# Optimization experiments

Measured on AMD Instinct MI355X. Metric: run time of the kernel, lower is better.

Reference implementation:

```python
import jax, jax.numpy as jnp
import numpy as np

EPS = 1e-3  # tfa InstanceNormalization default epsilon
H = 4       # num_attention_heads


def _inorm(x, g, b, axes):
    # instance norm: normalize over the given (spatial) axes, affine per channel
    m = jnp.mean(x, axis=axes, keepdims=True)
    v = jnp.var(x, axis=axes, keepdims=True)
    return (x - m) * jax.lax.rsqrt(v + EPS) * g + b


def setup_inputs() -> dict:
    key = jax.random.key(0)
    ks = jax.random.split(key, 20)
    B, N, C, E = 1, 196, 480, 4  # batch, tokens, KV_size_C, embedding_channels
    d = {}
    for i, n in enumerate(['emb1', 'emb2', 'emb3', 'emb4']):
        d[n] = jax.random.normal(ks[i], (B, N, E), jnp.float32)
    d['emb_C'] = jax.random.normal(ks[4], (B, N, C), jnp.float32)
    for i, n in enumerate(['Wq_C', 'Wk_C', 'Wv_C']):
        d[n] = jax.random.normal(ks[5 + i], (C, C), jnp.float32) * 0.02
    for i, n in enumerate(['Wq1', 'Wq2', 'Wq3', 'Wq4', 'Wk', 'Wv', 'Wo1', 'Wo2', 'Wo3', 'Wo4']):
        d[n] = jax.random.normal(ks[8 + i], (E, E), jnp.float32) * 0.25
    d['g1'] = jnp.ones((), jnp.float32)   # psi1 gamma (single channel)
    d['b1'] = jnp.zeros((), jnp.float32)  # psi1 beta
    d['g2'] = jnp.ones((H,), jnp.float32)   # psi2 gamma (per head)
    d['b2'] = jnp.zeros((H,), jnp.float32)  # psi2 beta
    return d


def reference(emb1, emb2, emb3, emb4, emb_C, Wq_C, Wk_C, Wv_C,
              Wq1, Wq2, Wq3, Wq4, Wk, Wv, Wo1, Wo2, Wo3, Wo4,
              g1, b1, g2, b2):
    B, N, C = emb_C.shape
    # ---- channel attention over emb_C ----
    Qc = emb_C @ Wq_C
    Kc = emb_C @ Wk_C
    Vc = emb_C @ Wv_C
    attn = jnp.einsum('bnc,bnd->bcd', Qc, Kc)            # Q_C^T @ K_C  [B,C,C]
    attn = _inorm(attn, g1, b1, axes=(-2, -1))           # psi1: 1-channel instance norm
    sim = jax.nn.softmax(attn, axis=-1)                  # dropout inactive (inference)
    T_hat = jnp.einsum('bcd,bnd->bnc', sim, Vc)          # (sim @ V_C^T)^T  [B,N,C]
    # split into C//4 chunks of width 4 along channels, concat along tokens
    KV_S = T_hat.reshape(B, N, C // 4, 4).transpose(0, 2, 1, 3).reshape(B, (C // 4) * N, 4)

    def heads(x):  # [B,T,4] -> [B,H,T,1]
        return x.reshape(B, -1, H, 1).transpose(0, 2, 1, 3)

    K = heads(KV_S @ Wk)   # [B,H,M,1], M = N*C//4
    V = heads(KV_S @ Wv)
    gh = g2.reshape(1, H, 1, 1)
    bh = b2.reshape(1, H, 1, 1)

    def branch(emb, Wq, Wo):
        Q = heads(emb @ Wq)                                  # [B,H,Nq,1]
        a = jnp.einsum('bhqd,bhkd->bhqk', Q, K)              # [B,H,Nq,M]
        a = _inorm(a, gh, bh, axes=(-2, -1))                 # psi2: per-head instance norm
        a = jax.nn.softmax(a, axis=-1)
        c = jnp.einsum('bhqk,bhkd->bhqd', a, V)              # [B,H,Nq,1]
        c = c.transpose(0, 2, 1, 3).reshape(B, -1, H)        # [B,Nq,4] (= KV_size_S)
        return c @ Wo

    return (branch(emb1, Wq1, Wo1), branch(emb2, Wq2, Wo2),
            branch(emb3, Wq3, Wo3), branch(emb4, Wq4, Wo4))
```

## Files before the change

### kernel.cpp

```cpp
#include <hip/hip_runtime.h>
#include <hip/hip_bf16.h>
#include <math.h>

#define N_TOK 196
#define M_KV  23520
#define EPSN  1e-3f
#define LOG2E 1.44269504088896340736f

#define OFF_QC    0
#define OFF_KC    94080
#define OFF_VC    188160
#define OFF_ATTN  282240
#define OFF_KV    512640
#define OFF_SPART 700800
#define OFF_KPART 701056

__device__ __forceinline__ float fast_exp2(float x) {
#if __has_builtin(__builtin_amdgcn_exp2f)
    return __builtin_amdgcn_exp2f(x);
#else
    return exp2f(x);
#endif
}

#define GEMM_COMPUTE(AS, BS) \
    _Pragma("unroll") \
    for (int kk2 = 0; kk2 < 16; ++kk2) { \
        float4 av = *(const float4*)&AS[kk2][ty*4]; \
        float2 bv = *(const float2*)&BS[kk2][tx*2]; \
        a00 = fmaf(av.x, bv.x, a00); a01 = fmaf(av.x, bv.y, a01); \
        a10 = fmaf(av.y, bv.x, a10); a11 = fmaf(av.y, bv.y, a11); \
        a20 = fmaf(av.z, bv.x, a20); a21 = fmaf(av.z, bv.y, a21); \
        a30 = fmaf(av.w, bv.x, a30); a31 = fmaf(av.w, bv.y, a31); \
    }

#define COMBINE_ACCS(CMB) \
    if (kg == 1) { \
        CMB[ty*4+0][tx*2] = a00; CMB[ty*4+0][tx*2+1] = a01; \
        CMB[ty*4+1][tx*2] = a10; CMB[ty*4+1][tx*2+1] = a11; \
        CMB[ty*4+2][tx*2] = a20; CMB[ty*4+2][tx*2+1] = a21; \
        CMB[ty*4+3][tx*2] = a30; CMB[ty*4+3][tx*2+1] = a31; \
    } \
    __syncthreads(); \
    if (kg == 0) { \
        a00 += CMB[ty*4+0][tx*2]; a01 += CMB[ty*4+0][tx*2+1]; \
        a10 += CMB[ty*4+1][tx*2]; a11 += CMB[ty*4+1][tx*2+1]; \
        a20 += CMB[ty*4+2][tx*2]; a21 += CMB[ty*4+2][tx*2+1]; \
        a30 += CMB[ty*4+3][tx*2]; a31 += CMB[ty*4+3][tx*2+1]; \
    }

__global__ __launch_bounds__(512) void k_qkv(const float* __restrict__ embC,
                                             const float* __restrict__ Wq,
                                             const float* __restrict__ Wk,
                                             const float* __restrict__ Wv,
                                             float* __restrict__ ws) {
    int bid = blockIdx.x;
    int zi = bid / 60, rem = bid % 60;
    int m0 = (rem / 15) * 64, n0 = (rem % 15) * 32;
    const float* W = (zi == 0) ? Wq : (zi == 1 ? Wk : Wv);
    float* o = ws + zi * 94080;
    __shared__ float As[2][2][16][68];
    __shared__ float Bs[2][2][16][36];
    __shared__ float Cmb[64][33];
    int tid = threadIdx.x;
    int kg = tid >> 8, t = tid & 255;
    int ty = t >> 4, tx = t & 15;
    float a00=0,a01=0,a10=0,a11=0,a20=0,a21=0,a30=0,a31=0;
    const float4 z4 = make_float4(0,0,0,0);
    int mrow = t >> 2, kq = (t & 3) * 4;
    bool am = (m0 + mrow) < N_TOK;
    const float* aptr = embC + (m0 + mrow) * 480 + kg * 240 + kq;
    bool bact = t < 128;
    int kk = t >> 3, nq = (t & 7) * 4;
    const float* bptr = W + (kg * 240 + kk) * 480 + n0 + nq;
    const int NS = 15;
    float4 ra = am ? *(const float4*)(aptr) : z4;
    float4 rb = bact ? *(const float4*)(bptr) : z4;
    As[kg][0][kq+0][mrow]=ra.x; As[kg][0][kq+1][mrow]=ra.y;
    As[kg][0][kq+2][mrow]=ra.z; As[kg][0][kq+3][mrow]=ra.w;
    if (bact) *(float4*)&Bs[kg][0][kk][nq] = rb;
    ra = am ? *(const float4*)(aptr + 16) : z4;
    rb = bact ? *(const float4*)(bptr + 16*480) : z4;
    __syncthreads();
    for (int s = 0; s < NS; ++s) {
        int b = s & 1;
        float4 fa = z4, fb = z4;
        if (s + 2 < NS) {
            fa = am ? *(const float4*)(aptr + (s+2)*16) : z4;
            fb = bact ? *(const float4*)(bptr + (s+2)*16*480) : z4;
        }
        GEMM_COMPUTE(As[kg][b], Bs[kg][b]);
        if (s + 1 < NS) {
            int nb = b ^ 1;
            As[kg][nb][kq+0][mrow]=ra.x; As[kg][nb][kq+1][mrow]=ra.y;
            As[kg][nb][kq+2][mrow]=ra.z; As[kg][nb][kq+3][mrow]=ra.w;
            if (bact) *(float4*)&Bs[kg][nb][kk][nq] = rb;
        }
        __syncthreads();
        ra = fa; rb = fb;
    }
    COMBINE_ACCS(Cmb);
    if (kg == 0) {
        int m = m0 + ty*4, n = n0 + tx*2;
        if (m   < N_TOK) *(float2*)(o + (m  )*480 + n) = make_float2(a00, a01);
        if (m+1 < N_TOK) *(float2*)(o + (m+1)*480 + n) = make_float2(a10, a11);
        if (m+2 < N_TOK) *(float2*)(o + (m+2)*480 + n) = make_float2(a20, a21);
        if (m+3 < N_TOK) *(float2*)(o + (m+3)*480 + n) = make_float2(a30, a31);
    }
}

__global__ __launch_bounds__(512) void k_attn(const float* __restrict__ Qc,
                                              const float* __restrict__ Kc,
                                              float* __restrict__ attn,
                                              float* __restrict__ Spart) {
    __shared__ float As[2][2][16][68];
    __shared__ float Bs[2][2][16][36];
    __shared__ float Cmb[64][33];
    __shared__ float red[8][2];
    int tid = threadIdx.x;
    int kg = tid >> 8, t = tid & 255;
    int n0 = blockIdx.x * 32, m0 = blockIdx.y * 64;
    int ty = t >> 4, tx = t & 15;
    float a00=0,a01=0,a10=0,a11=0,a20=0,a21=0,a30=0,a31=0;
    const float4 z4 = make_float4(0,0,0,0);
    int kka = t >> 4, mq = (t & 15) * 4;
    bool amq = (m0 + mq) < 480;
    int kbase = kg * 112;
    const float* aptr = Qc + (kbase + kka) * 480 + m0 + mq;
    bool bact = t < 128;
    int kk = t >> 3, nq = (t & 7) * 4;
    const float* bptr = Kc + (kbase + kk) * 480 + n0 + nq;
    const int NS = 7;
    float4 ra = (amq && kbase + kka < N_TOK) ? *(const float4*)(aptr) : z4;
    float4 rb = (bact && kbase + kk < N_TOK) ? *(const float4*)(bptr) : z4;
    *(float4*)&As[kg][0][kka][mq] = ra;
    if (bact) *(float4*)&Bs[kg][0][kk][nq] = rb;
    ra = (amq && kbase + 16 + kka < N_TOK) ? *(const float4*)(aptr + 16*480) : z4;
    rb = (bact && kbase + 16 + kk < N_TOK) ? *(const float4*)(bptr + 16*480) : z4;
    __syncthreads();
    for (int s = 0; s < NS; ++s) {
        int b = s & 1;
        float4 fa = z4, fb = z4;
        if (s + 2 < NS) {
            int k0 = kbase + (s + 2) * 16;
            fa = (amq && k0 + kka < N_TOK) ? *(const float4*)(aptr + (s+2)*16*480) : z4;
            fb = (bact && k0 + kk < N_TOK) ? *(const float4*)(bptr + (s+2)*16*480) : z4;
        }
        GEMM_COMPUTE(As[kg][b], Bs[kg][b]);
        if (s + 1 < NS) {
            int nb = b ^ 1;
            *(float4*)&As[kg][nb][kka][mq] = ra;
            if (bact) *(float4*)&Bs[kg][nb][kk][nq] = rb;
        }
        __syncthreads();
        ra = fa; rb = fb;
    }
    COMBINE_ACCS(Cmb);
    float ls = 0.f, lq = 0.f;
    if (kg == 0) {
        int m = m0 + ty*4, n = n0 + tx*2;
        if (m   < 480) *(float2*)(attn + (m  )*480 + n) = make_float2(a00, a01);
        if (m+1 < 480) *(float2*)(attn + (m+1)*480 + n) = make_float2(a10, a11);
        if (m+2 < 480) *(float2*)(attn + (m+2)*480 + n) = make_float2(a20, a21);
        if (m+3 < 480) *(float2*)(attn + (m+3)*480 + n) = make_float2(a30, a31);
        ls = a00+a01+a10+a11+a20+a21+a30+a31;
        lq = a00*a00+a01*a01+a10*a10+a11*a11+a20*a20+a21*a21+a30*a30+a31*a31;
    }
    #pragma unroll
    for (int o = 32; o > 0; o >>= 1) { ls += __shfl_xor(ls, o, 64); lq += __shfl_xor(lq, o, 64); }
    int wid = tid >> 6, lane = tid & 63;
    if (lane == 0) { red[wid][0] = ls; red[wid][1] = lq; }
    __syncthreads();
    if (tid == 0) {
        int bid = blockIdx.y * gridDim.x + blockIdx.x;
        Spart[bid*2]   = red[0][0] + red[1][0] + red[2][0] + red[3][0];
        Spart[bid*2+1] = red[0][1] + red[1][1] + red[2][1] + red[3][1];
    }
}

__global__ __launch_bounds__(512) void k_thatkv(const float* __restrict__ Vc,
                                                const float* __restrict__ attn,
                                                const float* __restrict__ Spart,
                                                const float* __restrict__ g1,
                                                const float* __restrict__ Wk,
                                                const float* __restrict__ Wv,
                                                float2* __restrict__ KV,
                                                float* __restrict__ kpart) {
    __shared__ float As[2][2][16][68];
    __shared__ float Bs[2][2][16][36];
    __shared__ float red[8][16];
    __shared__ float colsum[32];
    __shared__ float Tile[64][33];
    int bid = blockIdx.x;
    int n0 = (bid % 15) * 32, m0 = (bid / 15) * 64;
    int tid = threadIdx.x;
    int kg = tid >> 8, t = tid & 255;
    int wid = tid >> 6, lane = tid & 63;
    if (tid < 32) colsum[tid] = 0.f;
    float ps = 0.f, pq = 0.f;
    if (tid < 120) { ps = Spart[tid*2]; pq = Spart[tid*2+1]; }
    #pragma unroll
    for (int o = 32; o > 0; o >>= 1) { ps += __shfl_xor(ps, o, 64); pq += __shfl_xor(pq, o, 64); }
    if (lane == 0) { red[wid][0] = ps; red[wid][1] = pq; }
    __syncthreads();
    float S = 0.f, SQ = 0.f;
    #pragma unroll
    for (int w = 0; w < 8; ++w) { S += red[w][0]; SQ += red[w][1]; }
    const float invCC = 1.f / (480.f * 480.f);
    float mean = S * invCC;
    float var  = SQ * invCC - mean * mean;
    float s2 = g1[0] * rsqrtf(var + EPSN) * LOG2E;
    int ty = t >> 4, tx = t & 15;
    float a00=0,a01=0,a10=0,a11=0,a20=0,a21=0,a30=0,a31=0;
    const float4 z4 = make_float4(0,0,0,0);
    int mrow = t >> 2, kq = (t & 3) * 4;
    bool am = (m0 + mrow) < N_TOK;
    const float* aptr = Vc + (m0 + mrow) * 480 + kg * 240 + kq;
    bool bact = t < 128;
    int nrow = t >> 2, bkq = (t & 3) * 4;
    const float* bptr = attn + (n0 + nrow) * 480 + kg * 240 + bkq;
    float bsum = 0.f;
    const int NS = 15;
    float4 ra = am ? *(const float4*)(aptr) : z4;
    float4 rb = bact ? *(const float4*)(bptr) : z4;
    As[kg][0][kq+0][mrow]=ra.x; As[kg][0][kq+1][mrow]=ra.y;
    As[kg][0][kq+2][mrow]=ra.z; As[kg][0][kq+3][mrow]=ra.w;
    if (bact) {
        float e0 = fast_exp2(s2 * rb.x), e1 = fast_exp2(s2 * rb.y);
        float e2 = fast_exp2(s2 * rb.z), e3 = fast_exp2(s2 * rb.w);
        Bs[kg][0][bkq+0][nrow] = e0; Bs[kg][0][bkq+1][nrow] = e1;
        Bs[kg][0][bkq+2][nrow] = e2; Bs[kg][0][bkq+3][nrow] = e3;
        bsum += e0 + e1 + e2 + e3;
    }
    ra = am ? *(const float4*)(aptr + 16) : z4;
    rb = bact ? *(const float4*)(bptr + 16) : z4;
    __syncthreads();
    for (int s = 0; s < NS; ++s) {
        int b = s & 1;
        float4 fa = z4, fb = z4;
        if (s + 2 < NS) {
            fa = am ? *(const float4*)(aptr + (s+2)*16) : z4;
            fb = bact ? *(const float4*)(bptr + (s+2)*16) : z4;
        }
        GEMM_COMPUTE(As[kg][b], Bs[kg][b]);
        if (s + 1 < NS) {
            int nb = b ^ 1;
            As[kg][nb][kq+0][mrow]=ra.x; As[kg][nb][kq+1][mrow]=ra.y;
            As[kg][nb][kq+2][mrow]=ra.z; As[kg][nb][kq+3][mrow]=ra.w;
            if (bact) {
                float e0 = fast_exp2(s2 * rb.x), e1 = fast_exp2(s2 * rb.y);
                float e2 = fast_exp2(s2 * rb.z), e3 = fast_exp2(s2 * rb.w);
                Bs[kg][nb][bkq+0][nrow] = e0; Bs[kg][nb][bkq+1][nrow] = e1;
                Bs[kg][nb][bkq+2][nrow] = e2; Bs[kg][nb][bkq+3][nrow] = e3;
                bsum += e0 + e1 + e2 + e3;
            }
        }
        __syncthreads();
        ra = fa; rb = fb;
    }
    if (bact) atomicAdd(&colsum[nrow], bsum);
    __syncthreads();
    if (tid < 32) colsum[tid] = 1.f / colsum[tid];
    int r0 = ty*4, cc = tx*2;
    if (kg == 1) {
        Tile[r0+0][cc] = a00; Tile[r0+0][cc+1] = a01;
        Tile[r0+1][cc] = a10; Tile[r0+1][cc+1] = a11;
        Tile[r0+2][cc] = a20; Tile[r0+2][cc+1] = a21;
        Tile[r0+3][cc] = a30; Tile[r0+3][cc+1] = a31;
    }
    __syncthreads();
    if (kg == 0) {
        float i0 = colsum[cc], i1 = colsum[cc+1];
        Tile[r0+0][cc] = (Tile[r0+0][cc] + a00) * i0; Tile[r0+0][cc+1] = (Tile[r0+0][cc+1] + a01) * i1;
        Tile[r0+1][cc] = (Tile[r0+1][cc] + a10) * i0; Tile[r0+1][cc+1] = (Tile[r0+1][cc+1] + a11) * i1;
        Tile[r0+2][cc] = (Tile[r0+2][cc] + a20) * i0; Tile[r0+2][cc+1] = (Tile[r0+2][cc+1] + a21) * i1;
        Tile[r0+3][cc] = (Tile[r0+3][cc] + a30) * i0; Tile[r0+3][cc+1] = (Tile[r0+3][cc+1] + a31) * i1;
    }
    __syncthreads();
    float su[4] = {0,0,0,0}, sq[4] = {0,0,0,0};
    {
        int e = tid;
        int tr = e >> 3, jj = e & 7;
        int tok = m0 + tr;
        bool act = tok < N_TOK;
        float c0 = Tile[tr][4*jj], c1 = Tile[tr][4*jj+1];
        float c2 = Tile[tr][4*jj+2], c3 = Tile[tr][4*jj+3];
        int m_kv = (n0/4 + jj) * 196 + tok;
        #pragma unroll
        for (int h = 0; h < 4; ++h) {
            float kh = c0*Wk[h] + c1*Wk[4+h] + c2*Wk[8+h] + c3*Wk[12+h];
            float vh = c0*Wv[h] + c1*Wv[4+h] + c2*Wv[8+h] + c3*Wv[12+h];
            if (act) {
                KV[h * M_KV + m_kv] = make_float2(kh, vh);
                su[h] += kh; sq[h] += kh * kh;
            }
        }
    }
    __syncthreads();
    #pragma unroll
    for (int h = 0; h < 4; ++h) {
        #pragma unroll
        for (int o = 32; o > 0; o >>= 1) {
            su[h] += __shfl_xor(su[h], o, 64);
            sq[h] += __shfl_xor(sq[h], o, 64);
        }
        if (lane == 0) { red[wid][h*2+0] = su[h]; red[wid][h*2+1] = sq[h]; }
    }
    __syncthreads();
    if (tid < 8) {
        int h = tid & 3, st = tid >> 2;
        float r = 0.f;
        #pragma unroll
        for (int w = 0; w < 8; ++w) r += red[w][h*2+st];
        kpart[st * 256 + h * 64 + bid] = r;
    }
}

#define QG 49
__global__ __launch_bounds__(1024) void k_branch(
        const float* __restrict__ emb1, const float* __restrict__ emb2,
        const float* __restrict__ emb3, const float* __restrict__ emb4,
        const float* __restrict__ Wq1, const float* __restrict__ Wq2,
        const float* __restrict__ Wq3, const float* __restrict__ Wq4,
        const float* __restrict__ g2v,
        const float2* __restrict__ KV, const float* __restrict__ kpart,
        const float* __restrict__ Wo1, const float* __restrict__ Wo2,
        const float* __restrict__ Wo3, const float* __restrict__ Wo4,
        float* __restrict__ out) {
    __shared__ float lsh[4][4][4];
    __shared__ float ash[4][4][4];
    int tid = threadIdx.x;
    int w = tid >> 6, lane = tid & 63;
    int h = w >> 2, p = w & 3;
    int bid = blockIdx.x;
    int i = bid / QG, qg = bid % QG;
    const float* emb = (i == 0) ? emb1 : (i == 1) ? emb2 : (i == 2) ? emb3 : emb4;
    const float* Wq  = (i == 0) ? Wq1 : (i == 1) ? Wq2 : (i == 2) ? Wq3 : Wq4;
    float wq0 = Wq[h], wq1 = Wq[4+h], wq2 = Wq[8+h], wq3 = Wq[12+h];
    float s = 0.f, s2 = 0.f;
    #pragma unroll
    for (int r = 0; r < 4; ++r) {
        int t = lane + r * 64;
        if (t < N_TOK) {
            float Q = emb[t*4]*wq0 + emb[t*4+1]*wq1 + emb[t*4+2]*wq2 + emb[t*4+3]*wq3;
            s += Q; s2 += Q * Q;
        }
    }
    float ks = 0.f, kq2 = 0.f;
    if (lane < 60) {
        ks  = kpart[0*256 + h*64 + lane];
        kq2 = kpart[1*256 + h*64 + lane];
    }
    #pragma unroll
    for (int o = 32; o > 0; o >>= 1) {
        s += __shfl_xor(s, o, 64); s2 += __shfl_xor(s2, o, 64);
        ks += __shfl_xor(ks, o, 64); kq2 += __shfl_xor(kq2, o, 64);
    }
    float Qbar = s * (1.f/196.f), Q2bar = s2 * (1.f/196.f);
    float Kbar = ks * (1.f/(float)M_KV), K2bar = kq2 * (1.f/(float)M_KV);
    float mu = Qbar * Kbar;
    float var = Q2bar * K2bar - mu * mu;
    float sc = g2v[h] * rsqrtf(var + EPSN);
    float B2[4];
    #pragma unroll
    for (int j = 0; j < 4; ++j) {
        int q = qg * 4 + j;
        float Qj = emb[q*4]*wq0 + emb[q*4+1]*wq1 + emb[q*4+2]*wq2 + emb[q*4+3]*wq3;
        B2[j] = Qj * sc * LOG2E;
    }
    const float4* kv4 = (const float4*)(KV + h * M_KV);
    const int KQ = M_KV / 8;
    int kstart = p * KQ, kendq = kstart + KQ;
    float l[4] = {0,0,0,0};
    float a[4] = {0,0,0,0};
#define PROC8(P) { \
        _Pragma("unroll") \
        for (int j = 0; j < 4; ++j) { \
            float x = fast_exp2(B2[j] * P.x); \
            l[j] += x; a[j] = fmaf(x, P.y, a[j]); \
            float y = fast_exp2(B2[j] * P.z); \
            l[j] += y; a[j] = fmaf(y, P.w, a[j]); \
        } }
    int k4 = kstart + lane;
    for (; k4 + 192 < kendq; k4 += 256) {
        float4 p0 = kv4[k4], p1 = kv4[k4+64], p2 = kv4[k4+128], p3 = kv4[k4+192];
        PROC8(p0); PROC8(p1); PROC8(p2); PROC8(p3);
    }
    for (; k4 < kendq; k4 += 64) { float4 pv = kv4[k4]; PROC8(pv); }
#undef PROC8
    #pragma unroll
    for (int j = 0; j < 4; ++j) {
        float lv = l[j], av = a[j];
        #pragma unroll
        for (int o = 32; o > 0; o >>= 1) { lv += __shfl_xor(lv, o, 64); av += __shfl_xor(av, o, 64); }
        if (lane == 0) { lsh[h][p][j] = lv; ash[h][p][j] = av; }
    }
    __syncthreads();
    if (tid < 4) {
        const float* Wo = (i == 0) ? Wo1 : (i == 1) ? Wo2 : (i == 2) ? Wo3 : Wo4;
        int j = tid;
        float c[4];
        #pragma unroll
        for (int hh = 0; hh < 4; ++hh) {
            float L = lsh[hh][0][j] + lsh[hh][1][j] + lsh[hh][2][j] + lsh[hh][3][j];
            float A = ash[hh][0][j] + ash[hh][1][j] + ash[hh][2][j] + ash[hh][3][j];
            c[hh] = A / L;
        }
        float4 o;
        o.x = c[0]*Wo[0] + c[1]*Wo[4] + c[2]*Wo[8]  + c[3]*Wo[12];
        o.y = c[0]*Wo[1] + c[1]*Wo[5] + c[2]*Wo[9]  + c[3]*Wo[13];
        o.z = c[0]*Wo[2] + c[1]*Wo[6] + c[2]*Wo[10] + c[3]*Wo[14];
        o.w = c[0]*Wo[3] + c[1]*Wo[7] + c[2]*Wo[11] + c[3]*Wo[15];
        *(float4*)(out + i * 784 + (qg * 4 + j) * 4) = o;
    }
}

extern "C" void kernel_launch(void* const* d_in, const int* in_sizes, int n_in,
                              void* d_out, int out_size, void* d_ws, size_t ws_size,
                              hipStream_t stream) {
    const float* emb1 = (const float*)d_in[0];
    const float* emb2 = (const float*)d_in[1];
    const float* emb3 = (const float*)d_in[2];
    const float* emb4 = (const float*)d_in[3];
    const float* embC = (const float*)d_in[4];
    const float* WqC  = (const float*)d_in[5];
    const float* WkC  = (const float*)d_in[6];
    const float* WvC  = (const float*)d_in[7];
    const float* Wq1  = (const float*)d_in[8];
    const float* Wq2  = (const float*)d_in[9];
    const float* Wq3  = (const float*)d_in[10];
    const float* Wq4  = (const float*)d_in[11];
    const float* Wk   = (const float*)d_in[12];
    const float* Wv   = (const float*)d_in[13];
    const float* Wo1  = (const float*)d_in[14];
    const float* Wo2  = (const float*)d_in[15];
    const float* Wo3  = (const float*)d_in[16];
    const float* Wo4  = (const float*)d_in[17];
    const float* g1   = (const float*)d_in[18];
    const float* g2   = (const float*)d_in[20];
    float* ws = (float*)d_ws;
    float* out = (float*)d_out;

    k_qkv<<<180, 512, 0, stream>>>(embC, WqC, WkC, WvC, ws);
    k_attn<<<dim3(15, 8), 512, 0, stream>>>(ws + OFF_QC, ws + OFF_KC,
                                            ws + OFF_ATTN, ws + OFF_SPART);
    k_thatkv<<<60, 512, 0, stream>>>(ws + OFF_VC, ws + OFF_ATTN, ws + OFF_SPART, g1,
                                     Wk, Wv, (float2*)(ws + OFF_KV), ws + OFF_KPART);
    k_branch<<<4 * QG, 1024, 0, stream>>>(emb1, emb2, emb3, emb4,
                                          Wq1, Wq2, Wq3, Wq4, g2,
                                          (const float2*)(ws + OFF_KV), ws + OFF_KPART,
                                          Wo1, Wo2, Wo3, Wo4, out);
}
```

Baseline: 64.87 us.

## Shrink attn and T_hat GEMM tiles to 32x32 to launch more blocks

The channel-attention GEMM and the T_hat/KV GEMM now use 32x32 output tiles with 2x2 per-thread micro-tiles instead of 64x32 with 4x2. This raises block counts from 120 to 225 and from 60 to 105, so more of the GPU's compute units are busy on these small problems. Partial-sum buffers, the workspace offsets and the reduction readers in k_thatkv and k_branch are resized to match. In exchange each thread does less work per shared-memory load and per-block sync, and the global loads are narrower.

```diff
diff --git a/kernel.cpp b/kernel.cpp
--- a/kernel.cpp
+++ b/kernel.cpp
@@ -13,7 +13,7 @@
 #define OFF_ATTN  282240
 #define OFF_KV    512640
 #define OFF_SPART 700800
-#define OFF_KPART 701056
+#define OFF_KPART 701312
 
 __device__ __forceinline__ float fast_exp2(float x) {
 #if __has_builtin(__builtin_amdgcn_exp2f)
@@ -23,7 +23,7 @@
 #endif
 }
 
-#define GEMM_COMPUTE(AS, BS) \
+#define GEMM_COMPUTE8(AS, BS) \
     _Pragma("unroll") \
     for (int kk2 = 0; kk2 < 16; ++kk2) { \
         float4 av = *(const float4*)&AS[kk2][ty*4]; \
@@ -34,19 +34,13 @@
         a30 = fmaf(av.w, bv.x, a30); a31 = fmaf(av.w, bv.y, a31); \
     }
 
-#define COMBINE_ACCS(CMB) \
-    if (kg == 1) { \
-        CMB[ty*4+0][tx*2] = a00; CMB[ty*4+0][tx*2+1] = a01; \
-        CMB[ty*4+1][tx*2] = a10; CMB[ty*4+1][tx*2+1] = a11; \
-        CMB[ty*4+2][tx*2] = a20; CMB[ty*4+2][tx*2+1] = a21; \
-        CMB[ty*4+3][tx*2] = a30; CMB[ty*4+3][tx*2+1] = a31; \
-    } \
-    __syncthreads(); \
-    if (kg == 0) { \
-        a00 += CMB[ty*4+0][tx*2]; a01 += CMB[ty*4+0][tx*2+1]; \
-        a10 += CMB[ty*4+1][tx*2]; a11 += CMB[ty*4+1][tx*2+1]; \
-        a20 += CMB[ty*4+2][tx*2]; a21 += CMB[ty*4+2][tx*2+1]; \
-        a30 += CMB[ty*4+3][tx*2]; a31 += CMB[ty*4+3][tx*2+1]; \
+#define GEMM_COMPUTE4(AS, BS) \
+    _Pragma("unroll") \
+    for (int kk2 = 0; kk2 < 16; ++kk2) { \
+        float2 av = *(const float2*)&AS[kk2][ty*2]; \
+        float2 bv = *(const float2*)&BS[kk2][tx*2]; \
+        a00 = fmaf(av.x, bv.x, a00); a01 = fmaf(av.x, bv.y, a01); \
+        a10 = fmaf(av.y, bv.x, a10); a11 = fmaf(av.y, bv.y, a11); \
     }
 
 __global__ __launch_bounds__(512) void k_qkv(const float* __restrict__ embC,
@@ -89,7 +83,7 @@
             fa = am ? *(const float4*)(aptr + (s+2)*16) : z4;
             fb = bact ? *(const float4*)(bptr + (s+2)*16*480) : z4;
         }
-        GEMM_COMPUTE(As[kg][b], Bs[kg][b]);
+        GEMM_COMPUTE8(As[kg][b], Bs[kg][b]);
         if (s + 1 < NS) {
             int nb = b ^ 1;
             As[kg][nb][kq+0][mrow]=ra.x; As[kg][nb][kq+1][mrow]=ra.y;
@@ -99,8 +93,18 @@
         __syncthreads();
         ra = fa; rb = fb;
     }
-    COMBINE_ACCS(Cmb);
+    if (kg == 1) {
+        Cmb[ty*4+0][tx*2] = a00; Cmb[ty*4+0][tx*2+1] = a01;
+        Cmb[ty*4+1][tx*2] = a10; Cmb[ty*4+1][tx*2+1] = a11;
+        Cmb[ty*4+2][tx*2] = a20; Cmb[ty*4+2][tx*2+1] = a21;
+        Cmb[ty*4+3][tx*2] = a30; Cmb[ty*4+3][tx*2+1] = a31;
+    }
+    __syncthreads();
     if (kg == 0) {
+        a00 += Cmb[ty*4+0][tx*2]; a01 += Cmb[ty*4+0][tx*2+1];
+        a10 += Cmb[ty*4+1][tx*2]; a11 += Cmb[ty*4+1][tx*2+1];
+        a20 += Cmb[ty*4+2][tx*2]; a21 += Cmb[ty*4+2][tx*2+1];
+        a30 += Cmb[ty*4+3][tx*2]; a31 += Cmb[ty*4+3][tx*2+1];
         int m = m0 + ty*4, n = n0 + tx*2;
         if (m   < N_TOK) *(float2*)(o + (m  )*480 + n) = make_float2(a00, a01);
         if (m+1 < N_TOK) *(float2*)(o + (m+1)*480 + n) = make_float2(a10, a11);
@@ -113,58 +117,62 @@
                                               const float* __restrict__ Kc,
                                               float* __restrict__ attn,
                                               float* __restrict__ Spart) {
-    __shared__ float As[2][2][16][68];
+    __shared__ float As[2][2][16][36];
     __shared__ float Bs[2][2][16][36];
-    __shared__ float Cmb[64][33];
+    __shared__ float Cmb[32][33];
     __shared__ float red[8][2];
     int tid = threadIdx.x;
     int kg = tid >> 8, t = tid & 255;
-    int n0 = blockIdx.x * 32, m0 = blockIdx.y * 64;
+    int n0 = blockIdx.x * 32, m0 = blockIdx.y * 32;
     int ty = t >> 4, tx = t & 15;
-    float a00=0,a01=0,a10=0,a11=0,a20=0,a21=0,a30=0,a31=0;
-    const float4 z4 = make_float4(0,0,0,0);
-    int kka = t >> 4, mq = (t & 15) * 4;
-    bool amq = (m0 + mq) < 480;
+    float a00=0,a01=0,a10=0,a11=0;
+    const float2 z2 = make_float2(0,0);
+    int kk = t >> 4, eq = (t & 15) * 2;
     int kbase = kg * 112;
-    const float* aptr = Qc + (kbase + kka) * 480 + m0 + mq;
-    bool bact = t < 128;
-    int kk = t >> 3, nq = (t & 7) * 4;
-    const float* bptr = Kc + (kbase + kk) * 480 + n0 + nq;
+    const float* aptr = Qc + kk * 480 + m0 + eq;
+    const float* bptr = Kc + kk * 480 + n0 + eq;
     const int NS = 7;
-    float4 ra = (amq && kbase + kka < N_TOK) ? *(const float4*)(aptr) : z4;
-    float4 rb = (bact && kbase + kk < N_TOK) ? *(const float4*)(bptr) : z4;
-    *(float4*)&As[kg][0][kka][mq] = ra;
-    if (bact) *(float4*)&Bs[kg][0][kk][nq] = rb;
-    ra = (amq && kbase + 16 + kka < N_TOK) ? *(const float4*)(aptr + 16*480) : z4;
-    rb = (bact && kbase + 16 + kk < N_TOK) ? *(const float4*)(bptr + 16*480) : z4;
+    float2 ra = (kbase + kk < N_TOK) ? *(const float2*)(aptr + kbase*480) : z2;
+    float2 rb = (kbase + kk < N_TOK) ? *(const float2*)(bptr + kbase*480) : z2;
+    *(float2*)&As[kg][0][kk][eq] = ra;
+    *(float2*)&Bs[kg][0][kk][eq] = rb;
+    bool v1 = (kbase + 16 + kk) < N_TOK;
+    ra = v1 ? *(const float2*)(aptr + (kbase+16)*480) : z2;
+    rb = v1 ? *(const float2*)(bptr + (kbase+16)*480) : z2;
     __syncthreads();
     for (int s = 0; s < NS; ++s) {
         int b = s & 1;
-        float4 fa = z4, fb = z4;
+        float2 fa = z2, fb = z2;
         if (s + 2 < NS) {
             int k0 = kbase + (s + 2) * 16;
-            fa = (amq && k0 + kka < N_TOK) ? *(const float4*)(aptr + (s+2)*16*480) : z4;
-            fb = (bact && k0 + kk < N_TOK) ? *(const float4*)(bptr + (s+2)*16*480) : z4;
-        }
-        GEMM_COMPUTE(As[kg][b], Bs[kg][b]);
+            if (k0 + kk < N_TOK) {
+                fa = *(const float2*)(aptr + k0*480);
+                fb = *(const float2*)(bptr + k0*480);
+            }
+        }
+        GEMM_COMPUTE4(As[kg][b], Bs[kg][b]);
         if (s + 1 < NS) {
             int nb = b ^ 1;
-            *(float4*)&As[kg][nb][kka][mq] = ra;
-            if (bact) *(float4*)&Bs[kg][nb][kk][nq] = rb;
+            *(float2*)&As[kg][nb][kk][eq] = ra;
+            *(float2*)&Bs[kg][nb][kk][eq] = rb;
         }
         __syncthreads();
         ra = fa; rb = fb;
     }
-    COMBINE_ACCS(Cmb);
+    if (kg == 1) {
+        Cmb[ty*2+0][tx*2] = a00; Cmb[ty*2+0][tx*2+1] = a01;
+        Cmb[ty*2+1][tx*2] = a10; Cmb[ty*2+1][tx*2+1] = a11;
+    }
+    __syncthreads();
     float ls = 0.f, lq = 0.f;
     if (kg == 0) {
-        int m = m0 + ty*4, n = n0 + tx*2;
-        if (m   < 480) *(float2*)(attn + (m  )*480 + n) = make_float2(a00, a01);
-        if (m+1 < 480) *(float2*)(attn + (m+1)*480 + n) = make_float2(a10, a11);
-        if (m+2 < 480) *(float2*)(attn + (m+2)*480 + n) = make_float2(a20, a21);
-        if (m+3 < 480) *(float2*)(attn + (m+3)*480 + n) = make_float2(a30, a31);
-        ls = a00+a01+a10+a11+a20+a21+a30+a31;
-        lq = a00*a00+a01*a01+a10*a10+a11*a11+a20*a20+a21*a21+a30*a30+a31*a31;
+        a00 += Cmb[ty*2+0][tx*2]; a01 += Cmb[ty*2+0][tx*2+1];
+        a10 += Cmb[ty*2+1][tx*2]; a11 += Cmb[ty*2+1][tx*2+1];
+        int m = m0 + ty*2, n = n0 + tx*2;
+        *(float2*)(attn + (m  )*480 + n) = make_float2(a00, a01);
+        *(float2*)(attn + (m+1)*480 + n) = make_float2(a10, a11);
+        ls = a00+a01+a10+a11;
+        lq = a00*a00+a01*a01+a10*a10+a11*a11;
     }
     #pragma unroll
     for (int o = 32; o > 0; o >>= 1) { ls += __shfl_xor(ls, o, 64); lq += __shfl_xor(lq, o, 64); }
@@ -173,8 +181,11 @@
     __syncthreads();
     if (tid == 0) {
         int bid = blockIdx.y * gridDim.x + blockIdx.x;
-        Spart[bid*2]   = red[0][0] + red[1][0] + red[2][0] + red[3][0];
-        Spart[bid*2+1] = red[0][1] + red[1][1] + red[2][1] + red[3][1];
+        float S = 0.f, SQ = 0.f;
+        #pragma unroll
+        for (int w = 0; w < 8; ++w) { S += red[w][0]; SQ += red[w][1]; }
+        Spart[bid*2]   = S;
+        Spart[bid*2+1] = SQ;
     }
 }
 
@@ -186,101 +197,88 @@
                                                 const float* __restrict__ Wv,
                                                 float2* __restrict__ KV,
                                                 float* __restrict__ kpart) {
-    __shared__ float As[2][2][16][68];
+    __shared__ float As[2][2][16][36];
     __shared__ float Bs[2][2][16][36];
-    __shared__ float red[8][16];
+    __shared__ float Cmb[32][33];
+    __shared__ float Tile[32][33];
+    __shared__ float red[8][8];
     __shared__ float colsum[32];
-    __shared__ float Tile[64][33];
     int bid = blockIdx.x;
-    int n0 = (bid % 15) * 32, m0 = (bid / 15) * 64;
+    int n0 = (bid % 15) * 32, m0 = (bid / 15) * 32;
     int tid = threadIdx.x;
     int kg = tid >> 8, t = tid & 255;
     int wid = tid >> 6, lane = tid & 63;
     if (tid < 32) colsum[tid] = 0.f;
     float ps = 0.f, pq = 0.f;
-    if (tid < 120) { ps = Spart[tid*2]; pq = Spart[tid*2+1]; }
+    if (tid < 225) { ps = Spart[tid*2]; pq = Spart[tid*2+1]; }
     #pragma unroll
     for (int o = 32; o > 0; o >>= 1) { ps += __shfl_xor(ps, o, 64); pq += __shfl_xor(pq, o, 64); }
-    if (lane == 0) { red[wid][0] = ps; red[wid][1] = pq; }
+    __shared__ float pr[8][2];
+    if (lane == 0) { pr[wid][0] = ps; pr[wid][1] = pq; }
     __syncthreads();
     float S = 0.f, SQ = 0.f;
     #pragma unroll
-    for (int w = 0; w < 8; ++w) { S += red[w][0]; SQ += red[w][1]; }
+    for (int w = 0; w < 8; ++w) { S += pr[w][0]; SQ += pr[w][1]; }
     const float invCC = 1.f / (480.f * 480.f);
     float mean = S * invCC;
     float var  = SQ * invCC - mean * mean;
     float s2 = g1[0] * rsqrtf(var + EPSN) * LOG2E;
     int ty = t >> 4, tx = t & 15;
-    float a00=0,a01=0,a10=0,a11=0,a20=0,a21=0,a30=0,a31=0;
-    const float4 z4 = make_float4(0,0,0,0);
-    int mrow = t >> 2, kq = (t & 3) * 4;
-    bool am = (m0 + mrow) < N_TOK;
-    const float* aptr = Vc + (m0 + mrow) * 480 + kg * 240 + kq;
-    bool bact = t < 128;
-    int nrow = t >> 2, bkq = (t & 3) * 4;
-    const float* bptr = attn + (n0 + nrow) * 480 + kg * 240 + bkq;
+    float a00=0,a01=0,a10=0,a11=0;
+    const float2 z2 = make_float2(0,0);
+    int mm = t >> 3, kq2 = (t & 7) * 2;
+    bool am = (m0 + mm) < N_TOK;
+    const float* aptr = Vc + (m0 + mm) * 480 + kg * 240 + kq2;
+    const float* bptr = attn + (n0 + mm) * 480 + kg * 240 + kq2;
     float bsum = 0.f;
     const int NS = 15;
-    float4 ra = am ? *(const float4*)(aptr) : z4;
-    float4 rb = bact ? *(const float4*)(bptr) : z4;
-    As[kg][0][kq+0][mrow]=ra.x; As[kg][0][kq+1][mrow]=ra.y;
-    As[kg][0][kq+2][mrow]=ra.z; As[kg][0][kq+3][mrow]=ra.w;
-    if (bact) {
+    float2 ra = am ? *(const float2*)(aptr) : z2;
+    float2 rb = *(const float2*)(bptr);
+    As[kg][0][kq2][mm] = ra.x; As[kg][0][kq2+1][mm] = ra.y;
+    {
         float e0 = fast_exp2(s2 * rb.x), e1 = fast_exp2(s2 * rb.y);
-        float e2 = fast_exp2(s2 * rb.z), e3 = fast_exp2(s2 * rb.w);
-        Bs[kg][0][bkq+0][nrow] = e0; Bs[kg][0][bkq+1][nrow] = e1;
-        Bs[kg][0][bkq+2][nrow] = e2; Bs[kg][0][bkq+3][nrow] = e3;
-        bsum += e0 + e1 + e2 + e3;
-    }
-    ra = am ? *(const float4*)(aptr + 16) : z4;
-    rb = bact ? *(const float4*)(bptr + 16) : z4;
+        Bs[kg][0][kq2][mm] = e0; Bs[kg][0][kq2+1][mm] = e1;
+        bsum += e0 + e1;
+    }
+    ra = am ? *(const float2*)(aptr + 16) : z2;
+    rb = *(const float2*)(bptr + 16);
     __syncthreads();
     for (int s = 0; s < NS; ++s) {
         int b = s & 1;
-        float4 fa = z4, fb = z4;
+        float2 fa = z2, fb = z2;
         if (s + 2 < NS) {
-            fa = am ? *(const float4*)(aptr + (s+2)*16) : z4;
-            fb = bact ? *(const float4*)(bptr + (s+2)*16) : z4;
-        }
-        GEMM_COMPUTE(As[kg][b], Bs[kg][b]);
+            fa = am ? *(const float2*)(aptr + (s+2)*16) : z2;
+            fb = *(const float2*)(bptr + (s+2)*16);
+        }
+        GEMM_COMPUTE4(As[kg][b], Bs[kg][b]);
         if (s + 1 < NS) {
             int nb = b ^ 1;
-            As[kg][nb][kq+0][mrow]=ra.x; As[kg][nb][kq+1][mrow]=ra.y;
-            As[kg][nb][kq+2][mrow]=ra.z; As[kg][nb][kq+3][mrow]=ra.w;
-            if (bact) {
-                float e0 = fast_exp2(s2 * rb.x), e1 = fast_exp2(s2 * rb.y);
-                float e2 = fast_exp2(s2 * rb.z), e3 = fast_exp2(s2 * rb.w);
-                Bs[kg][nb][bkq+0][nrow] = e0; Bs[kg][nb][bkq+1][nrow] = e1;
-                Bs[kg][nb][bkq+2][nrow] = e2; Bs[kg][nb][bkq+3][nrow] = e3;
-                bsum += e0 + e1 + e2 + e3;
-            }
+            As[kg][nb][kq2][mm] = ra.x; As[kg][nb][kq2+1][mm] = ra.y;
+            float e0 = fast_exp2(s2 * rb.x), e1 = fast_exp2(s2 * rb.y);
+            Bs[kg][nb][kq2][mm] = e0; Bs[kg][nb][kq2+1][mm] = e1;
+            bsum += e0 + e1;
         }
         __syncthreads();
         ra = fa; rb = fb;
     }
-    if (bact) atomicAdd(&colsum[nrow], bsum);
+    atomicAdd(&colsum[mm], bsum);
+    int r0 = ty*2, cc = tx*2;
+    if (kg == 1) {
+        Cmb[r0+0][cc] = a00; Cmb[r0+0][cc+1] = a01;
+        Cmb[r0+1][cc] = a10; Cmb[r0+1][cc+1] = a11;
+    }
     __syncthreads();
     if (tid < 32) colsum[tid] = 1.f / colsum[tid];
-    int r0 = ty*4, cc = tx*2;
-    if (kg == 1) {
-        Tile[r0+0][cc] = a00; Tile[r0+0][cc+1] = a01;
-        Tile[r0+1][cc] = a10; Tile[r0+1][cc+1] = a11;
-        Tile[r0+2][cc] = a20; Tile[r0+2][cc+1] = a21;
-        Tile[r0+3][cc] = a30; Tile[r0+3][cc+1] = a31;
-    }
     __syncthreads();
     if (kg == 0) {
         float i0 = colsum[cc], i1 = colsum[cc+1];
-        Tile[r0+0][cc] = (Tile[r0+0][cc] + a00) * i0; Tile[r0+0][cc+1] = (Tile[r0+0][cc+1] + a01) * i1;
-        Tile[r0+1][cc] = (Tile[r0+1][cc] + a10) * i0; Tile[r0+1][cc+1] = (Tile[r0+1][cc+1] + a11) * i1;
-        Tile[r0+2][cc] = (Tile[r0+2][cc] + a20) * i0; Tile[r0+2][cc+1] = (Tile[r0+2][cc+1] + a21) * i1;
-        Tile[r0+3][cc] = (Tile[r0+3][cc] + a30) * i0; Tile[r0+3][cc+1] = (Tile[r0+3][cc+1] + a31) * i1;
+        Tile[r0+0][cc] = (Cmb[r0+0][cc] + a00) * i0; Tile[r0+0][cc+1] = (Cmb[r0+0][cc+1] + a01) * i1;
+        Tile[r0+1][cc] = (Cmb[r0+1][cc] + a10) * i0; Tile[r0+1][cc+1] = (Cmb[r0+1][cc+1] + a11) * i1;
     }
     __syncthreads();
     float su[4] = {0,0,0,0}, sq[4] = {0,0,0,0};
-    {
-        int e = tid;
-        int tr = e >> 3, jj = e & 7;
+    if (tid < 256) {
+        int tr = tid >> 3, jj = tid & 7;
         int tok = m0 + tr;
         bool act = tok < N_TOK;
         float c0 = Tile[tr][4*jj], c1 = Tile[tr][4*jj+1];
@@ -312,7 +310,7 @@
         float r = 0.f;
         #pragma unroll
         for (int w = 0; w < 8; ++w) r += red[w][h*2+st];
-        kpart[st * 256 + h * 64 + bid] = r;
+        kpart[st * 512 + h * 128 + bid] = r;
     }
 }
 
@@ -340,17 +338,19 @@
     float s = 0.f, s2 = 0.f;
     #pragma unroll
     for (int r = 0; r < 4; ++r) {
-        int t = lane + r * 64;
-        if (t < N_TOK) {
-            float Q = emb[t*4]*wq0 + emb[t*4+1]*wq1 + emb[t*4+2]*wq2 + emb[t*4+3]*wq3;
+        int tt = lane + r * 64;
+        if (tt < N_TOK) {
+            float Q = emb[tt*4]*wq0 + emb[tt*4+1]*wq1 + emb[tt*4+2]*wq2 + emb[tt*4+3]*wq3;
             s += Q; s2 += Q * Q;
         }
     }
-    float ks = 0.f, kq2 = 0.f;
-    if (lane < 60) {
-        ks  = kpart[0*256 + h*64 + lane];
-        kq2 = kpart[1*256 + h*64 + lane];
-    }
+    float ks  = kpart[0*512 + h*128 + lane];
+    float kq2 = kpart[1*512 + h*128 + lane];
+    if (lane + 64 < 105) {
+        ks  += kpart[0*512 + h*128 + 64 + lane];
+        kq2 += kpart[1*512 + h*128 + 64 + lane];
+    }
+    if (lane >= 105) {  }
     #pragma unroll
     for (int o = 32; o > 0; o >>= 1) {
         s += __shfl_xor(s, o, 64); s2 += __shfl_xor(s2, o, 64);
@@ -442,10 +442,10 @@
     float* out = (float*)d_out;
 
     k_qkv<<<180, 512, 0, stream>>>(embC, WqC, WkC, WvC, ws);
-    k_attn<<<dim3(15, 8), 512, 0, stream>>>(ws + OFF_QC, ws + OFF_KC,
-                                            ws + OFF_ATTN, ws + OFF_SPART);
-    k_thatkv<<<60, 512, 0, stream>>>(ws + OFF_VC, ws + OFF_ATTN, ws + OFF_SPART, g1,
-                                     Wk, Wv, (float2*)(ws + OFF_KV), ws + OFF_KPART);
+    k_attn<<<dim3(15, 15), 512, 0, stream>>>(ws + OFF_QC, ws + OFF_KC,
+                                             ws + OFF_ATTN, ws + OFF_SPART);
+    k_thatkv<<<105, 512, 0, stream>>>(ws + OFF_VC, ws + OFF_ATTN, ws + OFF_SPART, g1,
+                                      Wk, Wv, (float2*)(ws + OFF_KV), ws + OFF_KPART);
     k_branch<<<4 * QG, 1024, 0, stream>>>(emb1, emb2, emb3, emb4,
                                           Wq1, Wq2, Wq3, Wq4, g2,
                                           (const float2*)(ws + OFF_KV), ws + OFF_KPART,
```

Result: faster. 62.21 us (-4.1%).
